# Optimization experiments

Measured on AMD Instinct MI355X. Metric: run time of the kernel, lower is better.

## Reference

```python
import jax, jax.numpy as jnp
import numpy as np

IMG = 640.0  # pixel coordinate range for keypoints


def setup_inputs() -> dict:
    key = jax.random.key(0)
    ks = jax.random.split(key, 16)
    B, N, M, C, D, G = 4, 4096, 4096, 256, 256, 32
    s = 1.0 / np.sqrt(C)
    inp = {
        "nodes_t": jax.random.normal(ks[0], (B, N, C), jnp.float32),
        "nodes_t1": jax.random.normal(ks[1], (B, M, C), jnp.float32),
        "kpts_t1_pred": jax.random.uniform(ks[2], (B, N, 2), jnp.float32) * IMG,
        "kpts_t1_actual": jax.random.uniform(ks[3], (B, M, 2), jnp.float32) * IMG,
        "Wq": jax.random.normal(ks[4], (D, C), jnp.float32) * s,
        "bq": jnp.zeros((D,), jnp.float32),
        "Wk": jax.random.normal(ks[5], (D, C), jnp.float32) * s,
        "bk": jnp.zeros((D,), jnp.float32),
        "Wv": jax.random.normal(ks[6], (D, C), jnp.float32) * s,
        "bv": jnp.zeros((D,), jnp.float32),
        "Wm": jax.random.normal(ks[7], (D, D), jnp.float32) * (1.0 / np.sqrt(D)),
        "bm": jnp.zeros((D,), jnp.float32),
        "Wg1": jax.random.normal(ks[8], (G, 3), jnp.float32) * (1.0 / np.sqrt(3.0)),
        "bg1": jnp.zeros((G,), jnp.float32),
        "Wg2": jax.random.normal(ks[9], (G, G), jnp.float32) * (1.0 / np.sqrt(G)),
        "bg2": jnp.zeros((G,), jnp.float32),
        "iter_idx": 0,
    }
    return inp


def reference(nodes_t, nodes_t1, kpts_t1_pred, kpts_t1_actual,
              Wq, bq, Wk, bk, Wv, bv, Wm, bm, Wg1, bg1, Wg2, bg2, iter_idx):
    # window size schedule (iter_idx is a static Python int)
    win = 64.0 if iter_idx == 0 else max(4.0, 32.0 / 2 ** (iter_idx - 1))

    Q = nodes_t @ Wq.T + bq      # [B,N,256]
    K = nodes_t1 @ Wk.T + bk     # [B,M,256]
    V = nodes_t1 @ Wv.T + bv     # [B,M,256]

    # distance-based window mask [B,N,M]
    du = jnp.abs(kpts_t1_pred[:, :, 0:1] - kpts_t1_actual[:, None, :, 0])
    dv = jnp.abs(kpts_t1_pred[:, :, 1:2] - kpts_t1_actual[:, None, :, 1])
    mask = (du < win) & (dv < win)

    attn = jnp.einsum('bnd,bmd->bnm', Q, K) / jnp.sqrt(jnp.float32(256.0))
    attn = jnp.where(mask, attn, jnp.float32(-1e9))
    w = jax.nn.softmax(attn, axis=-1)

    matched_features = jnp.einsum('bnm,bmd->bnd', w, V)        # [B,N,256]
    matched_kpts = jnp.einsum('bnm,bmc->bnc', w, kpts_t1_actual)  # [B,N,2]

    confidence = jnp.any(mask, axis=-1, keepdims=True).astype(jnp.float32)  # [B,N,1]
    flow_residual = (matched_kpts - kpts_t1_pred) * confidence

    geo_in = jnp.concatenate([flow_residual, confidence], axis=-1)  # [B,N,3]
    h = jax.nn.silu(geo_in @ Wg1.T + bg1)
    geo_temp = h @ Wg2.T + bg2                                   # [B,N,32]

    merged = matched_features @ Wm.T + bm                        # [B,N,256]
    return merged, geo_temp, flow_residual, confidence
```

## Files before the change

kernel.cpp:

```cpp
#include <hip/hip_runtime.h>
#include <hip/hip_bf16.h>

typedef unsigned short ushort;
typedef unsigned int uint;
typedef __bf16 bf16x8 __attribute__((ext_vector_type(8)));
typedef float f32x4 __attribute__((ext_vector_type(4)));
typedef ushort ushort8 __attribute__((ext_vector_type(8)));

#define LOG2E 1.4426950408889634f
#define MFMA16(a,b,c) __builtin_amdgcn_mfma_f32_16x16x32_bf16((a),(b),(c),0,0,0)
#define GLL16(src, dst) __builtin_amdgcn_global_load_lds( \
    (const __attribute__((address_space(1))) void*)(src), \
    (__attribute__((address_space(3))) void*)(dst), 16, 0, 0)
#define GLL4(src, dst) __builtin_amdgcn_global_load_lds( \
    (const __attribute__((address_space(1))) void*)(src), \
    (__attribute__((address_space(3))) void*)(dst), 4, 0, 0)
#define SCHED0() __builtin_amdgcn_sched_barrier(0)

static __device__ __forceinline__ uint packbf(float lo, float hi) {
  union { __bf16 h[2]; uint u; } x;
  x.h[0] = (__bf16)lo; x.h[1] = (__bf16)hi;
  return x.u;
}
static __device__ __forceinline__ int cellof(float x) {
  int c = (int)(x * 0.015625f);
  return c < 0 ? 0 : (c > 9 ? 9 : c);
}

__global__ __launch_bounds__(256) void prep_kernel(
    const float* __restrict__ Wq, const float* __restrict__ Wk,
    const float* __restrict__ Wv, const float* __restrict__ Wm,
    __bf16* __restrict__ wsW,
    const float* __restrict__ n0, const float* __restrict__ n1,
    __bf16* __restrict__ a0, __bf16* __restrict__ a1,
    const float* __restrict__ kpred, const float* __restrict__ kact,
    int* __restrict__ hist, int* __restrict__ cellpt,
    float* __restrict__ meanN)
{
  const int bid = blockIdx.x, tid = threadIdx.x;
  if (bid < 64) {
    const int which = bid >> 4;
    const float* src = which == 0 ? Wq : which == 1 ? Wk : which == 2 ? Wv : Wm;
    const int i = (bid & 15) * 4096 + tid * 16;
    #pragma unroll
    for (int j2 = 0; j2 < 4; j2++) {
      f32x4 v = *(const f32x4*)(src + i + j2 * 4);
      union { __bf16 h[4]; uint u[2]; } x;
      #pragma unroll
      for (int j = 0; j < 4; j++) x.h[j] = (__bf16)v[j];
      *(uint*)(wsW + (size_t)which * 65536 + i + j2 * 4) = x.u[0];
      *(uint*)(wsW + (size_t)which * 65536 + i + j2 * 4 + 2) = x.u[1];
    }
  } else if (bid < 8256) {
    const int k = bid - 64;
    const float* s = k < 4096 ? n0 : n1;
    __bf16* o = k < 4096 ? a0 : a1;
    const int i = (k & 4095) * 1024 + tid * 4;
    f32x4 v = *(const f32x4*)(s + i);
    union { __bf16 h[4]; uint u[2]; } x;
    #pragma unroll
    for (int j = 0; j < 4; j++) x.h[j] = (__bf16)v[j];
    *(uint*)(o + i) = x.u[0];
    *(uint*)(o + i + 2) = x.u[1];
  } else if (bid < 8384) {
    const int p = (bid - 8256) * 256 + tid;
    const int type = p >> 14, idx = p & 16383;
    const float2 c = ((const float2*)(type == 0 ? kpred : kact))[idx];
    const int cell = cellof(c.x) * 10 + cellof(c.y);
    const int b = idx >> 12;
    atomicAdd(&hist[(type * 4 + b) * 128 + cell], 1);
    cellpt[type * 16384 + idx] = cell;
  } else {
    const int mb = bid - 8384;
    const int b = mb >> 4, chunk = mb & 15;
    const float* base = n1 + ((size_t)b * 4096 + chunk * 256) * 256 + tid;
    float s = 0.f;
    for (int r = 0; r < 256; r++) s += base[(size_t)r * 256];
    atomicAdd(&meanN[b * 256 + tid], s);
  }
}

__global__ __launch_bounds__(256) void scan_vmean(
    const int* __restrict__ hist, int* __restrict__ strt, int* __restrict__ curs,
    const float* __restrict__ meanN, const float* __restrict__ Wv,
    const float* __restrict__ bv, float* __restrict__ Vmean)
{
  __shared__ int sh[1024];
  __shared__ float mn[256];
  const int t = threadIdx.x;
  if (blockIdx.x == 0) {
    for (int i = t; i < 1024; i += 256) sh[i] = hist[i];
    __syncthreads();
    if (t < 8) {
      int run = 0;
      for (int c = 0; c < 100; c++) {
        strt[t * 128 + c] = run;
        curs[t * 128 + c] = run;
        run += sh[t * 128 + c];
      }
      strt[t * 128 + 100] = run;
    }
  } else {
    const int b = blockIdx.x - 1;
    mn[t] = meanN[b * 256 + t] * (1.0f / 4096.0f);
    __syncthreads();
    float s = bv[t];
    const float* w = Wv + (size_t)t * 256;
    for (int c = 0; c < 256; c++) s += mn[c] * w[c];
    Vmean[b * 256 + t] = s;
  }
}

__global__ __launch_bounds__(256) void scatter_kernel(
    const float* __restrict__ kpred, const float* __restrict__ kact,
    const int* __restrict__ cellpt, int* __restrict__ curs,
    int* __restrict__ sq, int* __restrict__ invq, float* __restrict__ kpS,
    int* __restrict__ sk, int* __restrict__ invk, float* __restrict__ kaS)
{
  int p = blockIdx.x * 256 + threadIdx.x;
  int type = p >> 14, idx = p & 16383;
  int b = idx >> 12, n = idx & 4095;
  int cell = cellpt[type * 16384 + idx];
  int pos = atomicAdd(&curs[(type * 4 + b) * 128 + cell], 1);
  if (type == 0) {
    sq[b * 4096 + pos] = n;
    invq[b * 4096 + n] = pos;
    ((float2*)kpS)[b * 4096 + pos] = ((const float2*)kpred)[idx];
  } else {
    sk[b * 4096 + pos] = n;
    invk[b * 4096 + n] = pos;
    ((float2*)kaS)[b * 4096 + pos] = ((const float2*)kact)[idx];
  }
}

__global__ __launch_bounds__(256) void gemm_qkv(
    const ushort* __restrict__ A0, const ushort* __restrict__ A1,
    const ushort* __restrict__ W4,
    const float* __restrict__ bq, const float* __restrict__ bk,
    const float* __restrict__ bv,
    __bf16* __restrict__ outQ, __bf16* __restrict__ outK,
    __bf16* __restrict__ outVs,
    const int* __restrict__ invq, const int* __restrict__ invk)
{
  const int z = blockIdx.z;
  const ushort* A = z == 0 ? A0 : A1;
  const ushort* Wa = z == 0 ? W4 : W4 + 65536;
  const ushort* Wb = W4 + 131072;
  const int* inv = z == 0 ? invq : invk;

  const int wid = threadIdx.x >> 6;
  const int lane = threadIdx.x & 63;
  const int q = lane & 15, g = lane >> 4;
  const int nb = blockIdx.x * 64 + (wid >> 1) * 32;
  const int db = blockIdx.y * 128 + (wid & 1) * 64;

  f32x4 acc[2][4], accv[2][4];
  #pragma unroll
  for (int a = 0; a < 2; a++)
    #pragma unroll
    for (int b = 0; b < 4; b++) {
      acc[a][b] = f32x4{0.f,0.f,0.f,0.f};
      accv[a][b] = f32x4{0.f,0.f,0.f,0.f};
    }

  const ushort* Wa0 = Wa + (size_t)(db + q) * 256 + g * 8;
  const ushort* Wb0 = Wb + (size_t)(db + q) * 256 + g * 8;
  const ushort* Ar0 = A + (size_t)(nb + q) * 256 + g * 8;
  const ushort* Ar1 = A + (size_t)(nb + 16 + q) * 256 + g * 8;

  #pragma unroll
  for (int c0 = 0; c0 < 256; c0 += 32) {
    bf16x8 a0 = *(const bf16x8*)(Ar0 + c0);
    bf16x8 a1 = *(const bf16x8*)(Ar1 + c0);
    #pragma unroll
    for (int df = 0; df < 4; df++) {
      bf16x8 w = *(const bf16x8*)(Wa0 + df * 16 * 256 + c0);
      acc[0][df] = MFMA16(a0, w, acc[0][df]);
      acc[1][df] = MFMA16(a1, w, acc[1][df]);
    }
    if (z == 1) {
      #pragma unroll
      for (int df = 0; df < 4; df++) {
        bf16x8 w = *(const bf16x8*)(Wb0 + df * 16 * 256 + c0);
        accv[0][df] = MFMA16(a0, w, accv[0][df]);
        accv[1][df] = MFMA16(a1, w, accv[1][df]);
      }
    }
  }
  const float* biasA = z == 0 ? bq : bk;
  __bf16* oA = z == 0 ? outQ : outK;
  #pragma unroll
  for (int df = 0; df < 4; df++) {
    float ba = biasA[db + df * 16 + q];
    float bb = bv[db + df * 16 + q];
    #pragma unroll
    for (int nf = 0; nf < 2; nf++)
      #pragma unroll
      for (int r = 0; r < 4; r++) {
        int row = nb + nf * 16 + g * 4 + r;
        int d = db + df * 16 + q;
        int pos = inv[row];
        size_t orow = (size_t)(row & ~4095) + pos;
        oA[orow * 256 + d] = (__bf16)(acc[nf][df][r] + ba);
        if (z == 1)
          outVs[orow * 256 + d] = (__bf16)(accv[nf][df][r] + bb);
      }
  }
}

__global__ __launch_bounds__(256) void transpose_v(
    const ushort* __restrict__ Vs, ushort* __restrict__ VT)
{
  __shared__ ushort tile[64][76];
  const int b = blockIdx.z, rt = blockIdx.x, dt = blockIdx.y;
  const int tid = threadIdx.x;
  const ushort* src = Vs + ((size_t)b * 4096 + rt * 64) * 256 + dt * 64;
  #pragma unroll
  for (int i = 0; i < 2; i++) {
    int c = tid + i * 256;
    int r = c >> 3, dc = (c & 7) * 8;
    ushort8 v = *(const ushort8*)(src + (size_t)r * 256 + dc);
    #pragma unroll
    for (int j = 0; j < 8; j++) tile[r][dc + j] = v[j];
  }
  __syncthreads();
  ushort* dst = VT + ((size_t)b * 256 + dt * 64) * 4096 + rt * 64;
  #pragma unroll
  for (int i = 0; i < 2; i++) {
    int c = tid + i * 256;
    int d = c >> 3, rc = (c & 7) * 8;
    ushort8 v;
    #pragma unroll
    for (int j = 0; j < 8; j++) v[j] = tile[rc + j][d];
    *(ushort8*)(dst + (size_t)d * 4096 + rc) = v;
  }
}

__global__ __launch_bounds__(256, 2) void attn_kernel(
    const ushort* __restrict__ Q,
    const ushort* __restrict__ K,
    const ushort* __restrict__ VT,
    const float* __restrict__ kpS,
    const int* __restrict__ iter_idx,
    const int* __restrict__ sq,
    const int* __restrict__ strt,
    const float* __restrict__ kaS,
    const float* __restrict__ Vmean,
    __bf16* __restrict__ matched,
    float* __restrict__ out_flow, float* __restrict__ out_conf)
{
  __shared__ __align__(16) ushort Kl[2][8192];
  __shared__ __align__(16) ushort Vl[2][8192];
  __shared__ __align__(16) float2 Cl[2][32];
  __shared__ int tl_t[132], tl_ks[132], tl_ke[132];
  __shared__ int ntile_s;

  const int tid = threadIdx.x;
  const int wid = tid >> 6, lane = tid & 63;
  const int q = lane & 15, g = lane >> 4;
  const int orig = blockIdx.x;
  const int wgid = (orig & 7) * 50 + (orig >> 3);
  const int batch = wgid / 100;
  const int cell = wgid % 100;

  const int qstart = strt[batch * 128 + cell];
  const int nq = strt[batch * 128 + cell + 1] - qstart;
  if (nq == 0) return;

  const int cu = cell / 10, cv = cell % 10;
  const int c0 = cv > 0 ? cv - 1 : 0, c1 = cv < 9 ? cv + 1 : 9;
  const int* kst = strt + (4 + batch) * 128;

  if (tid == 0) {
    int n = 0;
    int lo = cu > 0 ? cu - 1 : 0, hi = cu < 9 ? cu + 1 : 9;
    for (int cc = lo; cc <= hi; cc++) {
      int ks = kst[cc * 10 + c0];
      int ke = kst[cc * 10 + c1 + 1];
      for (int t = ks & ~31; t < ke; t += 32) {
        tl_t[n] = t; tl_ks[n] = ks; tl_ke[n] = ke; n++;
      }
    }
    ntile_s = n;
  }
  __syncthreads();
  const int ntile = ntile_s;

  const int idx = *iter_idx;
  const float win = (idx == 0) ? 64.0f : fmaxf(4.0f, ldexpf(32.0f, 1 - idx));

  const ushort* Kbase = K + (size_t)batch * 4096 * 256;
  const ushort* VTb = VT + (size_t)batch * 1048576;
  const float* kasf = kaS + (size_t)batch * 8192;
  const float* Vm = Vmean + batch * 256;

  const int npass = (nq + 63) >> 6;

  auto STAGE_K = [&](int ti, int b) {
    const int t = tl_t[ti];
    #pragma unroll
    for (int j = 0; j < 4; j++) {
      int n = wid * 256 + j * 64 + lane;
      int r = n >> 5, u = n & 31;
      GLL16(Kbase + (size_t)(t + r) * 256 + ((u ^ (r & 7)) * 8),
            &Kl[b][(size_t)(wid * 256 + j * 64) * 8]);
    }
    if (wid == 0) GLL4(kasf + t * 2 + lane, &Cl[b][0]);
  };
  auto STAGE_V = [&](int ti, int b) {
    const int t = tl_t[ti];
    #pragma unroll
    for (int j = 0; j < 4; j++) {
      int n = wid * 256 + j * 64 + lane;
      int d = n >> 2, c = n & 3;
      GLL16(VTb + (size_t)d * 4096 + t + ((c ^ ((d >> 1) & 3)) * 8),
            &Vl[b][(size_t)(wid * 256 + j * 64) * 8]);
    }
  };

  int cnt = 0, qi = 0, qbase_s = 0;
  bool active = false;
  float pu = 0.f, pv = 0.f;
  bf16x8 qf[8];
  f32x4 O[16];
  float m_run = -1e9f, l_run = 0.f, u_run = 0.f, v_run = 0.f;

  auto PASS_INIT = [&](int pp) {
    int tbase = pp * 64 + wid * 16;
    active = tbase < nq;
    cnt = active ? min(16, nq - tbase) : 0;
    qbase_s = batch * 4096 + qstart + tbase;
    if (active) {
      int qq = q < cnt ? q : cnt - 1;
      int qsrow = qbase_s + qq;
      qi = sq[qsrow];
      const ushort* qptr = Q + (size_t)qsrow * 256 + g * 8;
      #pragma unroll
      for (int mf = 0; mf < 8; mf++) qf[mf] = *(const bf16x8*)(qptr + mf * 32);
      float2 kpv = ((const float2*)kpS)[qsrow];
      pu = kpv.x; pv = kpv.y;
    }
    #pragma unroll
    for (int i = 0; i < 16; i++) O[i] = f32x4{0.f,0.f,0.f,0.f};
    m_run = -1e9f; l_run = 0.f; u_run = 0.f; v_run = 0.f;
  };

  auto EPILOGUE = [&]() {
    if (!active) return;
    l_run += __shfl_xor(l_run, 16); l_run += __shfl_xor(l_run, 32);
    u_run += __shfl_xor(u_run, 16); u_run += __shfl_xor(u_run, 32);
    v_run += __shfl_xor(v_run, 16); v_run += __shfl_xor(v_run, 32);
    bool degen = (m_run <= -5e8f) || (l_run == 0.f);
    float rinv = degen ? 0.f : 1.0f / l_run;
    if (g == 0 && q < cnt) {
      float conf = degen ? 0.f : 1.0f;
      int row = batch * 4096 + qi;
      float fu = (u_run * rinv - pu) * conf, fv = (v_run * rinv - pv) * conf;
      ((float2*)out_flow)[row] = float2{fu, fv};
      out_conf[row] = conf;
    }
    #pragma unroll
    for (int r = 0; r < 4; r++) {
      int slot = 4 * g + r;
      float il_r = __shfl(rinv, slot);
      bool dg_r = (il_r == 0.f);
      if (slot < cnt) {
        __bf16* mrow = matched + (size_t)(qbase_s + slot) * 256;
        #pragma unroll
        for (int df = 0; df < 16; df++) {
          float val = dg_r ? Vm[df * 16 + q] : O[df][r] * il_r;
          mrow[df * 16 + q] = (__bf16)val;
        }
      }
    }
  };

  if (ntile == 0) {
    for (int pp = 0; pp < npass; pp++) { PASS_INIT(pp); EPILOGUE(); }
    return;
  }

  const int total = npass * ntile;
  STAGE_K(0, 0);
  STAGE_V(0, 0);
  PASS_INIT(0);

  int i = 0, pp = 0;
  for (int it = 0; it < total; ++it) {
    const int b = it & 1;
    const int ni = (i + 1 == ntile) ? 0 : i + 1;
    const bool more = (it + 1 < total);
    const int nb = (it + 1) & 1;

    asm volatile("s_waitcnt vmcnt(4)" ::: "memory");
    SCHED0();
    __builtin_amdgcn_s_barrier();
    SCHED0();
    if (more) STAGE_K(ni, nb);

    const int t = tl_t[i], ks = tl_ks[i], ke = tl_ke[i];
    float sv[8], aus[8], avs[8];
    uint pp0 = 0, pp1 = 0, pp2 = 0, pp3 = 0;

    if (active) {
      f32x4 s0a = {0.f,0.f,0.f,0.f}, s0b = {0.f,0.f,0.f,0.f};
      f32x4 s1a = {0.f,0.f,0.f,0.f}, s1b = {0.f,0.f,0.f,0.f};
      __builtin_amdgcn_s_setprio(1);
      #pragma unroll
      for (int mf = 0; mf < 8; mf += 2) {
        const int u0 = (mf * 4 + g) ^ (q & 7);
        const int u1 = ((mf + 1) * 4 + g) ^ (q & 7);
        bf16x8 ka0 = *(const bf16x8*)&Kl[b][(size_t)(q * 32 + u0) * 8];
        bf16x8 kb0 = *(const bf16x8*)&Kl[b][(size_t)(q * 32 + u1) * 8];
        bf16x8 ka1 = *(const bf16x8*)&Kl[b][(size_t)((q + 16) * 32 + u0) * 8];
        bf16x8 kb1 = *(const bf16x8*)&Kl[b][(size_t)((q + 16) * 32 + u1) * 8];
        s0a = MFMA16(ka0, qf[mf],     s0a);
        s0b = MFMA16(kb0, qf[mf + 1], s0b);
        s1a = MFMA16(ka1, qf[mf],     s1a);
        s1b = MFMA16(kb1, qf[mf + 1], s1b);
      }
      __builtin_amdgcn_s_setprio(0);

      #pragma unroll
      for (int r = 0; r < 4; r++) {
        int jr = t + 4 * g + r;
        float2 cc0 = Cl[b][4 * g + r];
        aus[r] = cc0.x; avs[r] = cc0.y;
        bool val = (jr >= ks && jr < ke);
        float du = fabsf(pu - cc0.x), dv = fabsf(pv - cc0.y);
        float sr = s0a[r] + s0b[r];
        sv[r] = (val && fmaxf(du, dv) < win) ? sr * 0.0625f : -1e9f;

        int jr1 = jr + 16;
        float2 cc1 = Cl[b][16 + 4 * g + r];
        aus[4 + r] = cc1.x; avs[4 + r] = cc1.y;
        val = (jr1 >= ks && jr1 < ke);
        du = fabsf(pu - cc1.x); dv = fabsf(pv - cc1.y);
        sr = s1a[r] + s1b[r];
        sv[4 + r] = (val && fmaxf(du, dv) < win) ? sr * 0.0625f : -1e9f;
      }

      float mt = fmaxf(fmaxf(fmaxf(sv[0], sv[1]), fmaxf(sv[2], sv[3])),
                       fmaxf(fmaxf(sv[4], sv[5]), fmaxf(sv[6], sv[7])));
      mt = fmaxf(mt, __shfl_xor(mt, 16));
      mt = fmaxf(mt, __shfl_xor(mt, 32));
      if (__any(mt > m_run + 8.0f)) {
        float m_new = fmaxf(m_run, mt);
        float scale = exp2f((m_run - m_new) * LOG2E);
        l_run *= scale; u_run *= scale; v_run *= scale;
        float s_r[4];
        #pragma unroll
        for (int r = 0; r < 4; r++) s_r[r] = __shfl(scale, 4 * g + r);
        #pragma unroll
        for (int df = 0; df < 16; df++)
          #pragma unroll
          for (int r = 0; r < 4; r++) O[df][r] *= s_r[r];
        m_run = m_new;
      }

      float p[8];
      #pragma unroll
      for (int ii = 0; ii < 8; ii++) p[ii] = exp2f((sv[ii] - m_run) * LOG2E);
      #pragma unroll
      for (int ii = 0; ii < 8; ii++) {
        l_run += p[ii];
        u_run += p[ii] * aus[ii];
        v_run += p[ii] * avs[ii];
      }
      pp0 = packbf(p[0], p[1]); pp1 = packbf(p[2], p[3]);
      pp2 = packbf(p[4], p[5]); pp3 = packbf(p[6], p[7]);
    }

    if (more) { asm volatile("s_waitcnt vmcnt(4)" ::: "memory"); }
    else      { asm volatile("s_waitcnt vmcnt(0)" ::: "memory"); }
    SCHED0();
    __builtin_amdgcn_s_barrier();
    SCHED0();
    if (more) STAGE_V(ni, nb);

    if (active) {
      int srcA = q + ((g & 1) << 5);
      int srcB = srcA + 16;
      uint x0 = (uint)__shfl((int)pp0, srcA), x1 = (uint)__shfl((int)pp1, srcA);
      uint x2 = (uint)__shfl((int)pp0, srcB), x3 = (uint)__shfl((int)pp1, srcB);
      uint y0 = (uint)__shfl((int)pp2, srcA), y1 = (uint)__shfl((int)pp3, srcA);
      uint y2 = (uint)__shfl((int)pp2, srcB), y3 = (uint)__shfl((int)pp3, srcB);
      union { uint i4[4]; bf16x8 v; } af;
      bool lo = (g < 2);
      af.i4[0] = lo ? x0 : y0; af.i4[1] = lo ? x1 : y1;
      af.i4[2] = lo ? x2 : y2; af.i4[3] = lo ? x3 : y3;

      const int vs = g ^ ((q >> 1) & 3);
      __builtin_amdgcn_s_setprio(1);
      #pragma unroll
      for (int df = 0; df < 16; df++) {
        bf16x8 vfd = *(const bf16x8*)&Vl[b][(size_t)((df * 16 + q) * 4 + vs) * 8];
        O[df] = MFMA16(af.v, vfd, O[df]);
      }
      __builtin_amdgcn_s_setprio(0);
    }

    if (i == ntile - 1) {
      EPILOGUE();
      pp++;
      if (pp < npass) PASS_INIT(pp);
      i = 0;
    } else {
      i++;
    }
  }
}

__global__ __launch_bounds__(256) void merged_geo(
    const ushort* __restrict__ A, const ushort* __restrict__ W,
    const float* __restrict__ bias, float* __restrict__ out,
    const int* __restrict__ sq,
    const float* __restrict__ flow, const float* __restrict__ conf_in,
    const float* __restrict__ Wg1, const float* __restrict__ bg1,
    const float* __restrict__ Wg2, const float* __restrict__ bg2,
    float* __restrict__ out_geo)
{
  __shared__ float w1[32][3], b1[32], b2[32];
  __shared__ __align__(16) float w2[32][32];
  if (blockIdx.x < 512) {
    const int wid = threadIdx.x >> 6;
    const int lane = threadIdx.x & 63;
    const int q = lane & 15, g = lane >> 4;
    const int nb = (blockIdx.x >> 1) * 64 + (wid >> 1) * 32;
    const int db = (blockIdx.x & 1) * 128 + (wid & 1) * 64;

    f32x4 acc[2][4];
    #pragma unroll
    for (int a = 0; a < 2; a++)
      #pragma unroll
      for (int b = 0; b < 4; b++) acc[a][b] = f32x4{0.f,0.f,0.f,0.f};

    const ushort* W0 = W + (size_t)(db + q) * 256 + g * 8;
    const ushort* Ar0 = A + (size_t)(nb + q) * 256 + g * 8;
    const ushort* Ar1 = A + (size_t)(nb + 16 + q) * 256 + g * 8;

    #pragma unroll
    for (int c0 = 0; c0 < 256; c0 += 32) {
      bf16x8 a0 = *(const bf16x8*)(Ar0 + c0);
      bf16x8 a1 = *(const bf16x8*)(Ar1 + c0);
      #pragma unroll
      for (int df = 0; df < 4; df++) {
        bf16x8 w = *(const bf16x8*)(W0 + df * 16 * 256 + c0);
        acc[0][df] = MFMA16(a0, w, acc[0][df]);
        acc[1][df] = MFMA16(a1, w, acc[1][df]);
      }
    }
    #pragma unroll
    for (int df = 0; df < 4; df++) {
      float bval = bias[db + df * 16 + q];
      #pragma unroll
      for (int nf = 0; nf < 2; nf++)
        #pragma unroll
        for (int r = 0; r < 4; r++) {
          int row = nb + nf * 16 + g * 4 + r;
          int orow = (row & ~4095) + sq[row];
          out[(size_t)orow * 256 + db + df * 16 + q] = acc[nf][df][r] + bval;
        }
    }
  } else {
    const int tid = threadIdx.x;
    for (int i = tid; i < 96; i += 256) w1[i / 3][i % 3] = Wg1[i];
    if (tid < 32) { b1[tid] = bg1[tid]; b2[tid] = bg2[tid]; }
    for (int i = tid; i < 1024; i += 256) w2[i / 32][i % 32] = Wg2[i];
    __syncthreads();

    int row = (blockIdx.x - 512) * 256 + tid;
    float2 f = ((const float2*)flow)[row];
    float c = conf_in[row];
    float h[32];
    #pragma unroll
    for (int j = 0; j < 32; j++) {
      float x = w1[j][0] * f.x + w1[j][1] * f.y + w1[j][2] * c + b1[j];
      h[j] = x / (1.f + __expf(-x));
    }
    #pragma unroll
    for (int o = 0; o < 32; o += 2) {
      float s0 = b2[o], s1 = b2[o + 1];
      #pragma unroll
      for (int j = 0; j < 32; j += 4) {
        f32x4 wa = *(const f32x4*)&w2[o][j];
        f32x4 wb = *(const f32x4*)&w2[o + 1][j];
        s0 += wa[0]*h[j] + wa[1]*h[j+1] + wa[2]*h[j+2] + wa[3]*h[j+3];
        s1 += wb[0]*h[j] + wb[1]*h[j+1] + wb[2]*h[j+2] + wb[3]*h[j+3];
      }
      ((float2*)out_geo)[((size_t)row * 32 + o) >> 1] = float2{s0, s1};
    }
  }
}

extern "C" void kernel_launch(void* const* d_in, const int* in_sizes, int n_in,
                              void* d_out, int out_size, void* d_ws, size_t ws_size,
                              hipStream_t stream) {
  const float* nodes_t  = (const float*)d_in[0];
  const float* nodes_t1 = (const float*)d_in[1];
  const float* kpred    = (const float*)d_in[2];
  const float* kact     = (const float*)d_in[3];
  const float* Wq = (const float*)d_in[4];  const float* bq = (const float*)d_in[5];
  const float* Wk = (const float*)d_in[6];  const float* bk = (const float*)d_in[7];
  const float* Wv = (const float*)d_in[8];  const float* bv = (const float*)d_in[9];
  const float* Wm = (const float*)d_in[10]; const float* bm = (const float*)d_in[11];
  const float* Wg1= (const float*)d_in[12]; const float* bg1= (const float*)d_in[13];
  const float* Wg2= (const float*)d_in[14]; const float* bg2= (const float*)d_in[15];
  const int* iter = (const int*)d_in[16];

  float* out_merged = (float*)d_out;
  float* out_geo  = out_merged + 4 * 4096 * 256;
  float* out_flow = out_geo + 4 * 4096 * 32;
  float* out_conf = out_flow + 4 * 4096 * 2;

  ushort* wsQ   = (ushort*)d_ws;
  ushort* wsK   = wsQ + 4194304;
  ushort* wsVT  = wsK + 4194304;
  ushort* wsM   = wsVT + 4194304;
  ushort* wsW   = wsM + 4194304;
  float*  kaS   = (float*)(wsW + 262144);
  float*  kpS   = kaS + 32768;
  float*  Vmean = kpS + 32768;
  int*    hist  = (int*)(Vmean + 1024);
  float*  meanN = (float*)(hist + 1024);
  int*    strt  = (int*)(meanN + 1024);
  int*    curs  = strt + 1024;
  int*    cellpt= curs + 1024;
  int*    sq    = cellpt + 32768;
  int*    sk    = sq + 16384;
  int*    invk  = sk + 16384;
  int*    invq  = invk + 16384;
  ushort* wsA0  = (ushort*)(invq + 16384);
  ushort* wsA1  = wsA0 + 4194304;

  hipMemsetAsync(hist, 0, 8192, stream);

  prep_kernel<<<8448, 256, 0, stream>>>(Wq, Wk, Wv, Wm, (__bf16*)wsW,
                                        nodes_t, nodes_t1,
                                        (__bf16*)wsA0, (__bf16*)wsA1,
                                        kpred, kact, hist, cellpt, meanN);
  scan_vmean<<<5, 256, 0, stream>>>(hist, strt, curs, meanN, Wv, bv, Vmean);
  scatter_kernel<<<128, 256, 0, stream>>>(kpred, kact, cellpt, curs,
                                          sq, invq, kpS, sk, invk, kaS);
  dim3 qg(256, 2, 2);
  gemm_qkv<<<qg, 256, 0, stream>>>(wsA0, wsA1, wsW, bq, bk, bv,
                                   (__bf16*)wsQ, (__bf16*)wsK, (__bf16*)wsM,
                                   invq, invk);
  dim3 tg(64, 4, 4);
  transpose_v<<<tg, 256, 0, stream>>>(wsM, wsVT);
  attn_kernel<<<400, 256, 0, stream>>>(wsQ, wsK, wsVT, kpS, iter,
                                       sq, strt, kaS, Vmean,
                                       (__bf16*)wsM, out_flow, out_conf);
  merged_geo<<<576, 256, 0, stream>>>(wsM, wsW + 196608, bm, out_merged, sq,
                                      out_flow, out_conf,
                                      Wg1, bg1, Wg2, bg2, out_geo);
}
```

Measured before the change: 185.2 us.

## Fuse fp32-to-bf16 activation conversion into QKV GEMM and drop P shuffles

The prep kernel no longer converts nodes_t and nodes_t1 to bf16 in a separate pass. The QKV GEMM now loads the fp32 activations directly and converts them in registers, which removes a full write and re-read of two 4M-element bf16 buffers. In the attention PV step, the cross-lane shuffles that rearranged packed probabilities into the 16x16x32 MFMA operand layout are gone. Each lane instead feeds its own probabilities into two 16x16x16 bf16 MFMAs with matching 4-element V reads. The cost is twice as much fp32 activation traffic per GEMM tile and twice as many MFMA and LDS instructions in the PV loop.

```diff
diff --git a/kernel.cpp b/kernel.cpp
--- a/kernel.cpp
+++ b/kernel.cpp
@@ -4,6 +4,8 @@
 typedef unsigned short ushort;
 typedef unsigned int uint;
 typedef __bf16 bf16x8 __attribute__((ext_vector_type(8)));
+typedef __bf16 bf16x4 __attribute__((ext_vector_type(4)));
+typedef short s16x4 __attribute__((ext_vector_type(4)));
 typedef float f32x4 __attribute__((ext_vector_type(4)));
 typedef ushort ushort8 __attribute__((ext_vector_type(8)));
 
@@ -17,11 +19,16 @@
     (__attribute__((address_space(3))) void*)(dst), 4, 0, 0)
 #define SCHED0() __builtin_amdgcn_sched_barrier(0)
 
-static __device__ __forceinline__ uint packbf(float lo, float hi) {
-  union { __bf16 h[2]; uint u; } x;
-  x.h[0] = (__bf16)lo; x.h[1] = (__bf16)hi;
-  return x.u;
-}
+static __device__ __forceinline__ f32x4 mfma16x16(bf16x4 a, bf16x4 b, f32x4 c) {
+#if __has_builtin(__builtin_amdgcn_mfma_f32_16x16x16_bf16)
+  return __builtin_amdgcn_mfma_f32_16x16x16_bf16(a, b, c, 0, 0, 0);
+#else
+  union { bf16x4 h; s16x4 s; } ua, ub;
+  ua.h = a; ub.h = b;
+  return __builtin_amdgcn_mfma_f32_16x16x16bf16_1k(ua.s, ub.s, c, 0, 0, 0);
+#endif
+}
+
 static __device__ __forceinline__ int cellof(float x) {
   int c = (int)(x * 0.015625f);
   return c < 0 ? 0 : (c > 9 ? 9 : c);
@@ -31,8 +38,7 @@
     const float* __restrict__ Wq, const float* __restrict__ Wk,
     const float* __restrict__ Wv, const float* __restrict__ Wm,
     __bf16* __restrict__ wsW,
-    const float* __restrict__ n0, const float* __restrict__ n1,
-    __bf16* __restrict__ a0, __bf16* __restrict__ a1,
+    const float* __restrict__ n1,
     const float* __restrict__ kpred, const float* __restrict__ kact,
     int* __restrict__ hist, int* __restrict__ cellpt,
     float* __restrict__ meanN)
@@ -51,19 +57,8 @@
       *(uint*)(wsW + (size_t)which * 65536 + i + j2 * 4) = x.u[0];
       *(uint*)(wsW + (size_t)which * 65536 + i + j2 * 4 + 2) = x.u[1];
     }
-  } else if (bid < 8256) {
-    const int k = bid - 64;
-    const float* s = k < 4096 ? n0 : n1;
-    __bf16* o = k < 4096 ? a0 : a1;
-    const int i = (k & 4095) * 1024 + tid * 4;
-    f32x4 v = *(const f32x4*)(s + i);
-    union { __bf16 h[4]; uint u[2]; } x;
-    #pragma unroll
-    for (int j = 0; j < 4; j++) x.h[j] = (__bf16)v[j];
-    *(uint*)(o + i) = x.u[0];
-    *(uint*)(o + i + 2) = x.u[1];
-  } else if (bid < 8384) {
-    const int p = (bid - 8256) * 256 + tid;
+  } else if (bid < 192) {
+    const int p = (bid - 64) * 256 + tid;
     const int type = p >> 14, idx = p & 16383;
     const float2 c = ((const float2*)(type == 0 ? kpred : kact))[idx];
     const int cell = cellof(c.x) * 10 + cellof(c.y);
@@ -71,7 +66,7 @@
     atomicAdd(&hist[(type * 4 + b) * 128 + cell], 1);
     cellpt[type * 16384 + idx] = cell;
   } else {
-    const int mb = bid - 8384;
+    const int mb = bid - 192;
     const int b = mb >> 4, chunk = mb & 15;
     const float* base = n1 + ((size_t)b * 4096 + chunk * 256) * 256 + tid;
     float s = 0.f;
@@ -134,7 +129,7 @@
 }
 
 __global__ __launch_bounds__(256) void gemm_qkv(
-    const ushort* __restrict__ A0, const ushort* __restrict__ A1,
+    const float* __restrict__ nodes_t, const float* __restrict__ nodes_t1,
     const ushort* __restrict__ W4,
     const float* __restrict__ bq, const float* __restrict__ bk,
     const float* __restrict__ bv,
@@ -143,7 +138,7 @@
     const int* __restrict__ invq, const int* __restrict__ invk)
 {
   const int z = blockIdx.z;
-  const ushort* A = z == 0 ? A0 : A1;
+  const float* A = z == 0 ? nodes_t : nodes_t1;
   const ushort* Wa = z == 0 ? W4 : W4 + 65536;
   const ushort* Wb = W4 + 131072;
   const int* inv = z == 0 ? invq : invk;
@@ -165,13 +160,19 @@
 
   const ushort* Wa0 = Wa + (size_t)(db + q) * 256 + g * 8;
   const ushort* Wb0 = Wb + (size_t)(db + q) * 256 + g * 8;
-  const ushort* Ar0 = A + (size_t)(nb + q) * 256 + g * 8;
-  const ushort* Ar1 = A + (size_t)(nb + 16 + q) * 256 + g * 8;
 
   #pragma unroll
   for (int c0 = 0; c0 < 256; c0 += 32) {
-    bf16x8 a0 = *(const bf16x8*)(Ar0 + c0);
-    bf16x8 a1 = *(const bf16x8*)(Ar1 + c0);
+    const float* Ar0 = A + (size_t)(nb + q) * 256 + g * 8 + c0;
+    const float* Ar1 = A + (size_t)(nb + 16 + q) * 256 + g * 8 + c0;
+    f32x4 u0 = *(const f32x4*)Ar0, u1 = *(const f32x4*)(Ar0 + 4);
+    f32x4 w0 = *(const f32x4*)Ar1, w1 = *(const f32x4*)(Ar1 + 4);
+    bf16x8 a0, a1;
+    #pragma unroll
+    for (int j = 0; j < 4; j++) {
+      a0[j] = (__bf16)u0[j]; a0[4 + j] = (__bf16)u1[j];
+      a1[j] = (__bf16)w0[j]; a1[4 + j] = (__bf16)w1[j];
+    }
     #pragma unroll
     for (int df = 0; df < 4; df++) {
       bf16x8 w = *(const bf16x8*)(Wa0 + df * 16 * 256 + c0);
@@ -399,8 +400,7 @@
     if (more) STAGE_K(ni, nb);
 
     const int t = tl_t[i], ks = tl_ks[i], ke = tl_ke[i];
-    float sv[8], aus[8], avs[8];
-    uint pp0 = 0, pp1 = 0, pp2 = 0, pp3 = 0;
+    bf16x4 af0 = {}, af1 = {};
 
     if (active) {
       f32x4 s0a = {0.f,0.f,0.f,0.f}, s0b = {0.f,0.f,0.f,0.f};
@@ -421,6 +421,7 @@
       }
       __builtin_amdgcn_s_setprio(0);
 
+      float aus[8], avs[8], sv[8];
       #pragma unroll
       for (int r = 0; r < 4; r++) {
         int jr = t + 4 * g + r;
@@ -467,8 +468,11 @@
         u_run += p[ii] * aus[ii];
         v_run += p[ii] * avs[ii];
       }
-      pp0 = packbf(p[0], p[1]); pp1 = packbf(p[2], p[3]);
-      pp2 = packbf(p[4], p[5]); pp3 = packbf(p[6], p[7]);
+      #pragma unroll
+      for (int j = 0; j < 4; j++) {
+        af0[j] = (__bf16)p[j];
+        af1[j] = (__bf16)p[4 + j];
+      }
     }
 
     if (more) { asm volatile("s_waitcnt vmcnt(4)" ::: "memory"); }
@@ -479,23 +483,18 @@
     if (more) STAGE_V(ni, nb);
 
     if (active) {
-      int srcA = q + ((g & 1) << 5);
-      int srcB = srcA + 16;
-      uint x0 = (uint)__shfl((int)pp0, srcA), x1 = (uint)__shfl((int)pp1, srcA);
-      uint x2 = (uint)__shfl((int)pp0, srcB), x3 = (uint)__shfl((int)pp1, srcB);
-      uint y0 = (uint)__shfl((int)pp2, srcA), y1 = (uint)__shfl((int)pp3, srcA);
-      uint y2 = (uint)__shfl((int)pp2, srcB), y3 = (uint)__shfl((int)pp3, srcB);
-      union { uint i4[4]; bf16x8 v; } af;
-      bool lo = (g < 2);
-      af.i4[0] = lo ? x0 : y0; af.i4[1] = lo ? x1 : y1;
-      af.i4[2] = lo ? x2 : y2; af.i4[3] = lo ? x3 : y3;
-
-      const int vs = g ^ ((q >> 1) & 3);
+      const int sw_g0 = (g >> 1);
+      const int sw_g1 = 2 + (g >> 1);
+      const int off_g = (g & 1) * 4;
       __builtin_amdgcn_s_setprio(1);
       #pragma unroll
       for (int df = 0; df < 16; df++) {
-        bf16x8 vfd = *(const bf16x8*)&Vl[b][(size_t)((df * 16 + q) * 4 + vs) * 8];
-        O[df] = MFMA16(af.v, vfd, O[df]);
+        const int d = df * 16 + q;
+        const int sw = (d >> 1) & 3;
+        bf16x4 vf0 = *(const bf16x4*)&Vl[b][(size_t)(d * 32 + (sw_g0 ^ sw) * 8 + off_g)];
+        bf16x4 vf1 = *(const bf16x4*)&Vl[b][(size_t)(d * 32 + (sw_g1 ^ sw) * 8 + off_g)];
+        O[df] = mfma16x16(af0, vf0, O[df]);
+        O[df] = mfma16x16(af1, vf1, O[df]);
       }
       __builtin_amdgcn_s_setprio(0);
     }
@@ -630,20 +629,17 @@
   int*    sk    = sq + 16384;
   int*    invk  = sk + 16384;
   int*    invq  = invk + 16384;
-  ushort* wsA0  = (ushort*)(invq + 16384);
-  ushort* wsA1  = wsA0 + 4194304;
 
   hipMemsetAsync(hist, 0, 8192, stream);
 
-  prep_kernel<<<8448, 256, 0, stream>>>(Wq, Wk, Wv, Wm, (__bf16*)wsW,
-                                        nodes_t, nodes_t1,
-                                        (__bf16*)wsA0, (__bf16*)wsA1,
-                                        kpred, kact, hist, cellpt, meanN);
+  prep_kernel<<<256, 256, 0, stream>>>(Wq, Wk, Wv, Wm, (__bf16*)wsW,
+                                       nodes_t1, kpred, kact,
+                                       hist, cellpt, meanN);
   scan_vmean<<<5, 256, 0, stream>>>(hist, strt, curs, meanN, Wv, bv, Vmean);
   scatter_kernel<<<128, 256, 0, stream>>>(kpred, kact, cellpt, curs,
                                           sq, invq, kpS, sk, invk, kaS);
   dim3 qg(256, 2, 2);
-  gemm_qkv<<<qg, 256, 0, stream>>>(wsA0, wsA1, wsW, bq, bk, bv,
+  gemm_qkv<<<qg, 256, 0, stream>>>(nodes_t, nodes_t1, wsW, bq, bk, bv,
                                    (__bf16*)wsQ, (__bf16*)wsK, (__bf16*)wsM,
                                    invq, invk);
   dim3 tg(64, 4, 4);
```

Result: slower. 196.0 us (+5.9%).
